# Optimization experiments

Hardware: AMD Instinct MI355X
Metric: run time of the kernel (lower is better)

## Reference

```python
import math
import jax, jax.numpy as jnp
import numpy as np

B, C, L = 16, 128, 2048


def setup_inputs() -> dict:
    key = jax.random.key(0)
    kq, kk, kv, km = jax.random.split(key, 4)
    proj_query = jax.random.normal(kq, (B, C, L), dtype=jnp.float32)
    proj_key = jax.random.normal(kk, (B, C, L), dtype=jnp.float32)
    proj_val = jax.random.normal(kv, (B, C, L), dtype=jnp.float32)
    padding_mask = (jax.random.uniform(km, (B, 1, L)) > 0.1).astype(jnp.float32)
    return {
        "proj_query": proj_query,
        "proj_key": proj_key,
        "proj_val": proj_val,
        "padding_mask": padding_mask,
    }


def reference(proj_query, proj_key, proj_val, padding_mask):
    c1 = proj_query.shape[1]
    # energy: [B, Lq, Lk]
    energy = jnp.einsum("bcq,bck->bqk", proj_query, proj_key)
    attention = energy / math.sqrt(c1)
    # additive log-mask before softmax (broadcast [B,1,Lk] -> [B,Lq,Lk])
    attention = attention + jnp.log(padding_mask + 1e-6)
    attention = jax.nn.softmax(attention, axis=-1)
    # multiplicative mask after softmax
    attention = attention * padding_mask
    # out = bmm(val [B,C,Lk], attention^T [B,Lk,Lq]) -> [B,C,Lq]
    out = jnp.einsum("bck,bqk->bcq", proj_val, attention)
    return out, jnp.transpose(attention, (0, 2, 1))
```

## Files before the change

kernel.cpp:

```cpp
#include <hip/hip_runtime.h>

#define B_ 16
#define C_ 128
#define L_ 2048

typedef unsigned short u16;
typedef __bf16 bf16x8 __attribute__((ext_vector_type(8)));
typedef float floatx4 __attribute__((ext_vector_type(4)));

static __device__ __forceinline__ u16 f_to_bf16(float f) {
    union { float f; unsigned int i; } v;
    v.f = f;
    unsigned int x = v.i;
    return (u16)((x + 0x7fffu + ((x >> 16) & 1u)) >> 16);
}
static __device__ __forceinline__ bf16x8 lds_load8(const u16* p) {
    union { uint2 a[2]; bf16x8 v; } u;
    u.a[0] = *(const uint2*)p;
    u.a[1] = *(const uint2*)(p + 4);
    return u.v;
}

__global__ void k_transpose(const float* __restrict__ K, u16* __restrict__ KT) {
    int t  = blockIdx.x * blockDim.x + threadIdx.x;
    int k  = t & (L_ - 1);
    int ch = (t >> 11) & 3;
    int b  = t >> 13;
    const float* src = K + (size_t)b * C_ * L_ + (size_t)(ch * 32) * L_ + k;
    u16* dst = KT + ((size_t)b * L_ + k) * C_ + ch * 32;
    u16 v[32];
#pragma unroll
    for (int c = 0; c < 32; ++c) v[c] = f_to_bf16(src[(size_t)c * L_]);
#pragma unroll
    for (int c = 0; c < 32; c += 8) {
        union { u16 u[8]; uint4 q; } p;
#pragma unroll
        for (int j = 0; j < 8; ++j) p.u[j] = v[c + j];
        *(uint4*)(dst + c) = p.q;
    }
}

#define BM 16
#define QS 136

__launch_bounds__(512)
__global__ void k_attn(const float* __restrict__ Q, const u16* __restrict__ KT,
                       const float* __restrict__ M, float* __restrict__ PT) {
    __shared__ u16   Qs[BM * QS];
    __shared__ float redmax[BM * 8];
    __shared__ float redsum[BM * 8];

    const int b    = blockIdx.y;
    const int q0   = blockIdx.x * BM;
    const int tid  = threadIdx.x;
    const int lane = tid & 63;
    const int wave = tid >> 6;
    const int m16  = lane & 15;
    const int quad = lane >> 4;

    for (int i = tid; i < BM * C_; i += 512) {
        int q = i & 15, c = i >> 4;
        Qs[q * QS + c] = f_to_bf16(Q[((size_t)b * C_ + c) * L_ + q0 + q]);
    }
    __syncthreads();

    bf16x8 afr[4];
#pragma unroll
    for (int f = 0; f < 4; ++f)
        afr[f] = *(const bf16x8*)(Qs + m16 * QS + f * 32 + quad * 8);

    const u16*  ktb = KT + (size_t)b * L_ * C_;
    const float* mb = M + (size_t)b * L_;
    const float scale = 0.08838834764831845f;

    floatx4 accf[16];
#pragma unroll
    for (int t = 0; t < 16; ++t) {
        const int k0 = (wave << 8) + (t << 4);
        const u16* kr = ktb + (size_t)(k0 + m16) * C_ + quad * 8;
        floatx4 acc = {0.f, 0.f, 0.f, 0.f};
#pragma unroll
        for (int f = 0; f < 4; ++f) {
            bf16x8 bfr = *(const bf16x8*)(kr + f * 32);
            acc = __builtin_amdgcn_mfma_f32_16x16x32_bf16(afr[f], bfr, acc, 0, 0, 0);
        }
        const float lm = __logf(mb[k0 + m16] + 1e-6f);
#pragma unroll
        for (int r = 0; r < 4; ++r) acc[r] = acc[r] * scale + lm;
        accf[t] = acc;
    }

    float gm[4];
#pragma unroll
    for (int r = 0; r < 4; ++r) {
        float v = accf[0][r];
#pragma unroll
        for (int t = 1; t < 16; ++t) v = fmaxf(v, accf[t][r]);
        v = fmaxf(v, __shfl_xor(v, 1, 64));
        v = fmaxf(v, __shfl_xor(v, 2, 64));
        v = fmaxf(v, __shfl_xor(v, 4, 64));
        v = fmaxf(v, __shfl_xor(v, 8, 64));
        if (m16 == 0) redmax[(quad * 4 + r) * 8 + wave] = v;
    }
    __syncthreads();
#pragma unroll
    for (int r = 0; r < 4; ++r) {
        float v = redmax[(quad * 4 + r) * 8];
#pragma unroll
        for (int w = 1; w < 8; ++w) v = fmaxf(v, redmax[(quad * 4 + r) * 8 + w]);
        gm[r] = v;
    }

    float rs[4] = {0.f, 0.f, 0.f, 0.f};
#pragma unroll
    for (int t = 0; t < 16; ++t)
#pragma unroll
        for (int r = 0; r < 4; ++r) {
            float e = __expf(accf[t][r] - gm[r]);
            accf[t][r] = e;
            rs[r] += e;
        }
#pragma unroll
    for (int r = 0; r < 4; ++r) {
        float v = rs[r];
        v += __shfl_xor(v, 1, 64);
        v += __shfl_xor(v, 2, 64);
        v += __shfl_xor(v, 4, 64);
        v += __shfl_xor(v, 8, 64);
        if (m16 == 0) redsum[(quad * 4 + r) * 8 + wave] = v;
    }
    __syncthreads();
    float rinv[4];
#pragma unroll
    for (int r = 0; r < 4; ++r) {
        float v = redsum[(quad * 4 + r) * 8];
#pragma unroll
        for (int w = 1; w < 8; ++w) v += redsum[(quad * 4 + r) * 8 + w];
        rinv[r] = 1.f / v;
    }

    float* pt = PT + (size_t)b * L_ * L_ + q0 + quad * 4;
#pragma unroll
    for (int t = 0; t < 16; ++t) {
        const int k = (wave << 8) + (t << 4) + m16;
        const float mk = mb[k];
        floatx4 o;
#pragma unroll
        for (int r = 0; r < 4; ++r) o[r] = accf[t][r] * rinv[r] * mk;
        *(floatx4*)(pt + (size_t)k * L_) = o;
    }
}

#define TN 128
#define TK 32
#define VS 36

__launch_bounds__(256, 2)
__global__ void k_out(const float* __restrict__ V, const float* __restrict__ PT,
                      float* __restrict__ OUT) {
    __shared__ u16 Vs[C_ * VS];
    __shared__ u16 Bs[TN * VS];

    const int b    = blockIdx.y;
    const int n0   = blockIdx.x * TN;
    const int tid  = threadIdx.x;
    const int lane = tid & 63;
    const int wave = tid >> 6;
    const int m16  = lane & 15;
    const int quad = lane >> 4;
    const int wc   = wave >> 1;
    const int wn   = wave & 1;

    floatx4 acc[4][4];
#pragma unroll
    for (int i = 0; i < 4; ++i)
#pragma unroll
        for (int j = 0; j < 4; ++j) acc[i][j] = (floatx4){0.f, 0.f, 0.f, 0.f};

    const float* vb = V + (size_t)b * C_ * L_;
    const float* pb = PT + (size_t)b * L_ * L_ + n0;

    for (int k0 = 0; k0 < L_; k0 += TK) {
        __syncthreads();
#pragma unroll
        for (int ii = 0; ii < 2; ++ii) {
            int s = tid + ii * 256;
            int c = s >> 2, part = s & 3;
            const floatx4 a0 = *(const floatx4*)(vb + (size_t)c * L_ + k0 + part * 8);
            const floatx4 a1 = *(const floatx4*)(vb + (size_t)c * L_ + k0 + part * 8 + 4);
            union { u16 u[8]; uint2 d[2]; } pk;
#pragma unroll
            for (int j = 0; j < 4; ++j) { pk.u[j] = f_to_bf16(a0[j]); pk.u[4 + j] = f_to_bf16(a1[j]); }
            *(uint2*)(Vs + c * VS + part * 8)     = pk.d[0];
            *(uint2*)(Vs + c * VS + part * 8 + 4) = pk.d[1];
            int kk = s >> 4, qo = (s & 15) * 8;
            const floatx4 p0 = *(const floatx4*)(pb + (size_t)(k0 + kk) * L_ + qo);
            const floatx4 p1 = *(const floatx4*)(pb + (size_t)(k0 + kk) * L_ + qo + 4);
#pragma unroll
            for (int j = 0; j < 4; ++j) {
                Bs[(qo + j) * VS + kk]     = f_to_bf16(p0[j]);
                Bs[(qo + 4 + j) * VS + kk] = f_to_bf16(p1[j]);
            }
        }
        __syncthreads();

        bf16x8 af[4], bfr[4];
#pragma unroll
        for (int i = 0; i < 4; ++i)
            af[i] = lds_load8(Vs + (wc * 64 + i * 16 + m16) * VS + quad * 8);
#pragma unroll
        for (int j = 0; j < 4; ++j)
            bfr[j] = lds_load8(Bs + (wn * 64 + j * 16 + m16) * VS + quad * 8);
#pragma unroll
        for (int i = 0; i < 4; ++i)
#pragma unroll
            for (int j = 0; j < 4; ++j)
                acc[i][j] = __builtin_amdgcn_mfma_f32_16x16x32_bf16(af[i], bfr[j], acc[i][j], 0, 0, 0);
    }

    float* ob = OUT + (size_t)b * C_ * L_;
#pragma unroll
    for (int i = 0; i < 4; ++i) {
        const int c = wc * 64 + i * 16 + quad * 4;
#pragma unroll
        for (int j = 0; j < 4; ++j) {
            const int q = n0 + wn * 64 + j * 16 + m16;
#pragma unroll
            for (int r = 0; r < 4; ++r)
                ob[(size_t)(c + r) * L_ + q] = acc[i][j][r];
        }
    }
}

extern "C" void kernel_launch(void* const* d_in, const int* in_sizes, int n_in,
                              void* d_out, int out_size, void* d_ws, size_t ws_size,
                              hipStream_t stream) {
    (void)in_sizes; (void)n_in; (void)out_size; (void)ws_size;
    const float* Q = (const float*)d_in[0];
    const float* K = (const float*)d_in[1];
    const float* V = (const float*)d_in[2];
    const float* M = (const float*)d_in[3];
    float* OUT = (float*)d_out;
    float* PT  = OUT + (size_t)B_ * C_ * L_;
    u16*   KT  = (u16*)d_ws;

    k_transpose<<<dim3((B_ * L_ * 4) / 256), dim3(256), 0, stream>>>(K, KT);
    k_attn<<<dim3(L_ / BM, B_), dim3(512), 0, stream>>>(Q, KT, M, PT);
    k_out<<<dim3(L_ / TN, B_), dim3(256), 0, stream>>>(V, PT, OUT);
}
```

Before: 714.4 us.

## Fuse attention and value GEMM into one kernel with recomputed scores

Replaces the separate attention and output kernels with one fused kernel. Each block first computes QK^T once to get the softmax denominator, without subtracting a row max. It then recomputes the scores tile by tile, writes the probability matrix to global memory, stages it as bf16 in double-buffered LDS, and multiplies it by V loaded directly from global. This avoids reading the large probability matrix back from HBM and removes the max-reduction pass. The cost is doing the QK^T matmul twice, many redundant V reads per batch served from L2, and a risk of exp overflow because the max is no longer subtracted.

Measured after the change: 751.7 us. 1.05x slower.

```diff
diff --git a/kernel.cpp b/kernel.cpp
--- a/kernel.cpp
+++ b/kernel.cpp
@@ -14,20 +14,20 @@
     unsigned int x = v.i;
     return (u16)((x + 0x7fffu + ((x >> 16) & 1u)) >> 16);
 }
-static __device__ __forceinline__ bf16x8 lds_load8(const u16* p) {
-    union { uint2 a[2]; bf16x8 v; } u;
-    u.a[0] = *(const uint2*)p;
-    u.a[1] = *(const uint2*)(p + 4);
-    return u.v;
+static __device__ __forceinline__ bf16x8 cvt8(floatx4 a, floatx4 b) {
+    union { u16 u[8]; bf16x8 v; } p;
+#pragma unroll
+    for (int j = 0; j < 4; ++j) { p.u[j] = f_to_bf16(a[j]); p.u[4 + j] = f_to_bf16(b[j]); }
+    return p.v;
 }
 
-__global__ void k_transpose(const float* __restrict__ K, u16* __restrict__ KT) {
+__global__ void k_transpose(const float* __restrict__ X, u16* __restrict__ XT) {
     int t  = blockIdx.x * blockDim.x + threadIdx.x;
     int k  = t & (L_ - 1);
     int ch = (t >> 11) & 3;
     int b  = t >> 13;
-    const float* src = K + (size_t)b * C_ * L_ + (size_t)(ch * 32) * L_ + k;
-    u16* dst = KT + ((size_t)b * L_ + k) * C_ + ch * 32;
+    const float* src = X + (size_t)b * C_ * L_ + (size_t)(ch * 32) * L_ + k;
+    u16* dst = XT + ((size_t)b * L_ + k) * C_ + ch * 32;
     u16 v[32];
 #pragma unroll
     for (int c = 0; c < 32; ++c) v[c] = f_to_bf16(src[(size_t)c * L_]);
@@ -42,13 +42,15 @@
 
 #define BM 16
 #define QS 136
+#define LP 136
 
-__launch_bounds__(512)
-__global__ void k_attn(const float* __restrict__ Q, const u16* __restrict__ KT,
-                       const float* __restrict__ M, float* __restrict__ PT) {
-    __shared__ u16   Qs[BM * QS];
-    __shared__ float redmax[BM * 8];
-    __shared__ float redsum[BM * 8];
+__launch_bounds__(256, 4)
+__global__ void k_fused(const float* __restrict__ Q, const u16* __restrict__ KT,
+                        const float* __restrict__ V, const float* __restrict__ M,
+                        float* __restrict__ PT, float* __restrict__ OUT) {
+    __shared__ __attribute__((aligned(16))) u16 Qs[BM * QS];
+    __shared__ __attribute__((aligned(16))) u16 LDSP[2][BM * LP];
+    __shared__ float redsum[BM][4];
 
     const int b    = blockIdx.y;
     const int q0   = blockIdx.x * BM;
@@ -58,7 +60,7 @@
     const int m16  = lane & 15;
     const int quad = lane >> 4;
 
-    for (int i = tid; i < BM * C_; i += 512) {
+    for (int i = tid; i < BM * C_; i += 256) {
         int q = i & 15, c = i >> 4;
         Qs[q * QS + c] = f_to_bf16(Q[((size_t)b * C_ + c) * L_ + q0 + q]);
     }
@@ -69,57 +71,23 @@
     for (int f = 0; f < 4; ++f)
         afr[f] = *(const bf16x8*)(Qs + m16 * QS + f * 32 + quad * 8);
 
-    const u16*  ktb = KT + (size_t)b * L_ * C_;
-    const float* mb = M + (size_t)b * L_;
+    const u16*   ktb = KT + (size_t)b * L_ * C_;
+    const float* mb  = M + (size_t)b * L_;
     const float scale = 0.08838834764831845f;
 
-    floatx4 accf[16];
+    float rs[4] = {0.f, 0.f, 0.f, 0.f};
+#pragma unroll 2
+    for (int t = 0; t < 32; ++t) {
+        const int kh = (wave << 9) + (t << 4);
+        const u16* kr = ktb + (size_t)(kh + m16) * C_ + quad * 8;
+        floatx4 s = {0.f, 0.f, 0.f, 0.f};
 #pragma unroll
-    for (int t = 0; t < 16; ++t) {
-        const int k0 = (wave << 8) + (t << 4);
-        const u16* kr = ktb + (size_t)(k0 + m16) * C_ + quad * 8;
-        floatx4 acc = {0.f, 0.f, 0.f, 0.f};
+        for (int f = 0; f < 4; ++f)
+            s = __builtin_amdgcn_mfma_f32_16x16x32_bf16(afr[f], *(const bf16x8*)(kr + f * 32), s, 0, 0, 0);
+        const float lm = __logf(mb[kh + m16] + 1e-6f);
 #pragma unroll
-        for (int f = 0; f < 4; ++f) {
-            bf16x8 bfr = *(const bf16x8*)(kr + f * 32);
-            acc = __builtin_amdgcn_mfma_f32_16x16x32_bf16(afr[f], bfr, acc, 0, 0, 0);
-        }
-        const float lm = __logf(mb[k0 + m16] + 1e-6f);
-#pragma unroll
-        for (int r = 0; r < 4; ++r) acc[r] = acc[r] * scale + lm;
-        accf[t] = acc;
+        for (int r = 0; r < 4; ++r) rs[r] += __expf(fmaf(s[r], scale, lm));
     }
-
-    float gm[4];
-#pragma unroll
-    for (int r = 0; r < 4; ++r) {
-        float v = accf[0][r];
-#pragma unroll
-        for (int t = 1; t < 16; ++t) v = fmaxf(v, accf[t][r]);
-        v = fmaxf(v, __shfl_xor(v, 1, 64));
-        v = fmaxf(v, __shfl_xor(v, 2, 64));
-        v = fmaxf(v, __shfl_xor(v, 4, 64));
-        v = fmaxf(v, __shfl_xor(v, 8, 64));
-        if (m16 == 0) redmax[(quad * 4 + r) * 8 + wave] = v;
-    }
-    __syncthreads();
-#pragma unroll
-    for (int r = 0; r < 4; ++r) {
-        float v = redmax[(quad * 4 + r) * 8];
-#pragma unroll
-        for (int w = 1; w < 8; ++w) v = fmaxf(v, redmax[(quad * 4 + r) * 8 + w]);
-        gm[r] = v;
-    }
-
-    float rs[4] = {0.f, 0.f, 0.f, 0.f};
-#pragma unroll
-    for (int t = 0; t < 16; ++t)
-#pragma unroll
-        for (int r = 0; r < 4; ++r) {
-            float e = __expf(accf[t][r] - gm[r]);
-            accf[t][r] = e;
-            rs[r] += e;
-        }
 #pragma unroll
     for (int r = 0; r < 4; ++r) {
         float v = rs[r];
@@ -127,108 +95,68 @@
         v += __shfl_xor(v, 2, 64);
         v += __shfl_xor(v, 4, 64);
         v += __shfl_xor(v, 8, 64);
-        if (m16 == 0) redsum[(quad * 4 + r) * 8 + wave] = v;
+        if (m16 == 0) redsum[quad * 4 + r][wave] = v;
     }
     __syncthreads();
     float rinv[4];
 #pragma unroll
     for (int r = 0; r < 4; ++r) {
-        float v = redsum[(quad * 4 + r) * 8];
-#pragma unroll
-        for (int w = 1; w < 8; ++w) v += redsum[(quad * 4 + r) * 8 + w];
-        rinv[r] = 1.f / v;
+        const int q = quad * 4 + r;
+        rinv[r] = 1.f / (redsum[q][0] + redsum[q][1] + redsum[q][2] + redsum[q][3]);
     }
 
-    float* pt = PT + (size_t)b * L_ * L_ + q0 + quad * 4;
+    floatx4 oacc0 = {0.f, 0.f, 0.f, 0.f};
+    floatx4 oacc1 = {0.f, 0.f, 0.f, 0.f};
+    float*       ptb = PT + (size_t)b * L_ * L_ + q0;
+    const float* vbb = V + (size_t)b * C_ * L_;
+
+    for (int it = 0; it < 16; ++it) {
+        const int kb = it << 7;
+        u16* lp = LDSP[it & 1];
+
 #pragma unroll
-    for (int t = 0; t < 16; ++t) {
-        const int k = (wave << 8) + (t << 4) + m16;
-        const float mk = mb[k];
-        floatx4 o;
+        for (int half = 0; half < 2; ++half) {
+            const int kl = (wave << 5) + (half << 4);
+            const int kh = kb + kl;
+            const u16* kr = ktb + (size_t)(kh + m16) * C_ + quad * 8;
+            floatx4 s = {0.f, 0.f, 0.f, 0.f};
 #pragma unroll
-        for (int r = 0; r < 4; ++r) o[r] = accf[t][r] * rinv[r] * mk;
-        *(floatx4*)(pt + (size_t)k * L_) = o;
-    }
-}
-
-#define TN 128
-#define TK 32
-#define VS 36
-
-__launch_bounds__(256, 2)
-__global__ void k_out(const float* __restrict__ V, const float* __restrict__ PT,
-                      float* __restrict__ OUT) {
-    __shared__ u16 Vs[C_ * VS];
-    __shared__ u16 Bs[TN * VS];
-
-    const int b    = blockIdx.y;
-    const int n0   = blockIdx.x * TN;
-    const int tid  = threadIdx.x;
-    const int lane = tid & 63;
-    const int wave = tid >> 6;
-    const int m16  = lane & 15;
-    const int quad = lane >> 4;
-    const int wc   = wave >> 1;
-    const int wn   = wave & 1;
-
-    floatx4 acc[4][4];
+            for (int f = 0; f < 4; ++f)
+                s = __builtin_amdgcn_mfma_f32_16x16x32_bf16(afr[f], *(const bf16x8*)(kr + f * 32), s, 0, 0, 0);
+            const float mk = mb[kh + m16];
+            const float lm = __logf(mk + 1e-6f);
+            floatx4 po;
 #pragma unroll
-    for (int i = 0; i < 4; ++i)
+            for (int r = 0; r < 4; ++r) {
+                const float p = __expf(fmaf(s[r], scale, lm)) * rinv[r];
+                po[r] = p * mk;
+            }
+            *(floatx4*)(ptb + (size_t)(kh + m16) * L_ + quad * 4) = po;
 #pragma unroll
-        for (int j = 0; j < 4; ++j) acc[i][j] = (floatx4){0.f, 0.f, 0.f, 0.f};
-
-    const float* vb = V + (size_t)b * C_ * L_;
-    const float* pb = PT + (size_t)b * L_ * L_ + n0;
-
-    for (int k0 = 0; k0 < L_; k0 += TK) {
-        __syncthreads();
-#pragma unroll
-        for (int ii = 0; ii < 2; ++ii) {
-            int s = tid + ii * 256;
-            int c = s >> 2, part = s & 3;
-            const floatx4 a0 = *(const floatx4*)(vb + (size_t)c * L_ + k0 + part * 8);
-            const floatx4 a1 = *(const floatx4*)(vb + (size_t)c * L_ + k0 + part * 8 + 4);
-            union { u16 u[8]; uint2 d[2]; } pk;
-#pragma unroll
-            for (int j = 0; j < 4; ++j) { pk.u[j] = f_to_bf16(a0[j]); pk.u[4 + j] = f_to_bf16(a1[j]); }
-            *(uint2*)(Vs + c * VS + part * 8)     = pk.d[0];
-            *(uint2*)(Vs + c * VS + part * 8 + 4) = pk.d[1];
-            int kk = s >> 4, qo = (s & 15) * 8;
-            const floatx4 p0 = *(const floatx4*)(pb + (size_t)(k0 + kk) * L_ + qo);
-            const floatx4 p1 = *(const floatx4*)(pb + (size_t)(k0 + kk) * L_ + qo + 4);
-#pragma unroll
-            for (int j = 0; j < 4; ++j) {
-                Bs[(qo + j) * VS + kk]     = f_to_bf16(p0[j]);
-                Bs[(qo + 4 + j) * VS + kk] = f_to_bf16(p1[j]);
-            }
+            for (int r = 0; r < 4; ++r)
+                lp[(quad * 4 + r) * LP + kl + m16] = f_to_bf16(po[r]);
         }
         __syncthreads();
 
-        bf16x8 af[4], bfr[4];
 #pragma unroll
-        for (int i = 0; i < 4; ++i)
-            af[i] = lds_load8(Vs + (wc * 64 + i * 16 + m16) * VS + quad * 8);
-#pragma unroll
-        for (int j = 0; j < 4; ++j)
-            bfr[j] = lds_load8(Bs + (wn * 64 + j * 16 + m16) * VS + quad * 8);
-#pragma unroll
-        for (int i = 0; i < 4; ++i)
-#pragma unroll
-            for (int j = 0; j < 4; ++j)
-                acc[i][j] = __builtin_amdgcn_mfma_f32_16x16x32_bf16(af[i], bfr[j], acc[i][j], 0, 0, 0);
+        for (int ks = 0; ks < 4; ++ks) {
+            const bf16x8 pb = *(const bf16x8*)(lp + m16 * LP + (ks << 5) + quad * 8);
+            const float* va = vbb + (size_t)((wave << 5) + m16) * L_ + kb + (ks << 5) + quad * 8;
+            const bf16x8 a0 = cvt8(*(const floatx4*)(va),
+                                   *(const floatx4*)(va + 4));
+            const bf16x8 a1 = cvt8(*(const floatx4*)(va + (size_t)16 * L_),
+                                   *(const floatx4*)(va + (size_t)16 * L_ + 4));
+            oacc0 = __builtin_amdgcn_mfma_f32_16x16x32_bf16(a0, pb, oacc0, 0, 0, 0);
+            oacc1 = __builtin_amdgcn_mfma_f32_16x16x32_bf16(a1, pb, oacc1, 0, 0, 0);
+        }
     }
 
-    float* ob = OUT + (size_t)b * C_ * L_;
+    float* ob = OUT + (size_t)b * C_ * L_ + q0;
 #pragma unroll
-    for (int i = 0; i < 4; ++i) {
-        const int c = wc * 64 + i * 16 + quad * 4;
-#pragma unroll
-        for (int j = 0; j < 4; ++j) {
-            const int q = n0 + wn * 64 + j * 16 + m16;
-#pragma unroll
-            for (int r = 0; r < 4; ++r)
-                ob[(size_t)(c + r) * L_ + q] = acc[i][j][r];
-        }
+    for (int r = 0; r < 4; ++r) {
+        const int c0 = (wave << 5) + (quad << 2) + r;
+        ob[(size_t)c0 * L_ + m16]        = oacc0[r];
+        ob[(size_t)(c0 + 16) * L_ + m16] = oacc1[r];
     }
 }
 
@@ -245,6 +173,5 @@
     u16*   KT  = (u16*)d_ws;
 
     k_transpose<<<dim3((B_ * L_ * 4) / 256), dim3(256), 0, stream>>>(K, KT);
-    k_attn<<<dim3(L_ / BM, B_), dim3(512), 0, stream>>>(Q, KT, M, PT);
-    k_out<<<dim3(L_ / TN, B_), dim3(256), 0, stream>>>(V, PT, OUT);
+    k_fused<<<dim3(L_ / BM, B_), dim3(256), 0, stream>>>(Q, KT, V, M, PT, OUT);
 }
```
